# Kernel tuning notes

Measured on AMD Instinct MI355X. Metric: run time of the kernel, lower is better.

## Reference

```python
import jax, jax.numpy as jnp
import numpy as np

H = 4  # num_heads
EPS = 1e-5


def setup_inputs() -> dict:
    key = jax.random.key(0)
    ks = jax.random.split(key, 12)
    N, C, E = 4096, 128, 131072
    x = jax.random.normal(ks[0], (N, C), dtype=jnp.float32)
    edge_index = jax.random.randint(ks[1], (2, E), 0, N, dtype=jnp.int64)
    # guarantee every row has at least one neighbor (self-loops) to avoid NaN softmax rows
    loops = jnp.arange(N, dtype=jnp.int64)
    edge_index = edge_index.at[0, :N].set(loops).at[1, :N].set(loops)
    s = 1.0 / np.sqrt(C)
    def lin(k):
        kw, kb = jax.random.split(k)
        return (jax.random.uniform(kw, (C, C), jnp.float32, -s, s),
                jax.random.uniform(kb, (C,), jnp.float32, -s, s))
    wq, bq = lin(ks[2]); wk, bk = lin(ks[3]); wv, bv = lin(ks[4]); wo, bo = lin(ks[5])
    gamma = jnp.ones((C,), jnp.float32)
    beta = jnp.zeros((C,), jnp.float32)
    return {"x": x, "edge_index": edge_index, "wq": wq, "bq": bq, "wk": wk, "bk": bk,
            "wv": wv, "bv": bv, "wo": wo, "bo": bo, "gamma": gamma, "beta": beta}


def reference(x, edge_index, wq, bq, wk, bk, wv, bv, wo, bo, gamma, beta):
    N, C = x.shape
    D = C // H
    q = (x @ wq.T + bq).reshape(N, H, D)
    k = (x @ wk.T + bk).reshape(N, H, D)
    v = (x @ wv.T + bv).reshape(N, H, D)
    scores = jnp.einsum('nhd,mhd->nhm', q, k) / jnp.sqrt(jnp.float32(D))  # [N,H,N]
    row, col = edge_index
    mask = jnp.zeros((N, N), jnp.float32).at[row, col].set(1.0)
    scores = jnp.where(mask[:, None, :] == 0, -jnp.inf, scores)
    attn = jax.nn.softmax(scores, axis=-1)  # dropout is identity in eval
    out = jnp.einsum('nhm,mhd->nhd', attn, v).reshape(N, C)
    out = out @ wo.T + bo
    y = x + out
    mu = jnp.mean(y, axis=-1, keepdims=True)
    var = jnp.var(y, axis=-1, keepdims=True)
    return (y - mu) / jnp.sqrt(var + EPS) * gamma + beta
```

## Files before the change

### kernel.cpp

```cpp
#include <hip/hip_runtime.h>

typedef unsigned long long u64;

#define C_DIM 128
#define MAXN 128
#define WSTR (C_DIM + 4)

__global__ __launch_bounds__(512, 4) void build_qkv_kernel(
    const int* __restrict__ ei, int E, u64* __restrict__ bm, int wpr,
    const float* __restrict__ x,
    const float* __restrict__ wq, const float* __restrict__ bq,
    const float* __restrict__ wk, const float* __restrict__ bk,
    const float* __restrict__ wv, const float* __restrict__ bv,
    const float* __restrict__ wo, float* __restrict__ woT,
    float* __restrict__ qo, float* __restrict__ ko, float* __restrict__ vo)
{
    const int ROWS = 8;
    __shared__ float xs[ROWS][C_DIM];
    __shared__ float wt[C_DIM * WSTR];
    int t = threadIdx.x;
    int n0 = blockIdx.x * ROWS;
    int tid = blockIdx.x * 512 + t;
    int nth = gridDim.x * 512;

    if (tid < E) {
        int r = ei[tid], c = ei[E + tid];
        atomicOr(&bm[(size_t)r * wpr + (c >> 6)], 1ull << (c & 63));
    }
    for (int i = tid; i < C_DIM * C_DIM; i += nth) {
        int c = i >> 7, j = i & 127;
        woT[i] = wo[j * C_DIM + c];
    }

    if (t < 256) {
        int r = t >> 5, c4 = (t & 31) << 2;
        *(float4*)&xs[r][c4] = *(const float4*)(x + (size_t)(n0 + r) * C_DIM + c4);
    }
    int row = t >> 6;
    int jg  = t & 63;
    const float* Wp[3] = {wq, wk, wv};
    const float* Bp[3] = {bq, bk, bv};
    float*       Op[3] = {qo, ko, vo};
    for (int s = 0; s < 3; ++s) {
        __syncthreads();
        const float* W = Wp[s];
        #pragma unroll
        for (int i = 0; i < 8; ++i) {
            int g = t + i * 512;
            int j = g >> 5, c4 = (g & 31) << 2;
            *(float4*)&wt[j * WSTR + c4] = *(const float4*)(W + (size_t)j * C_DIM + c4);
        }
        __syncthreads();
        const float* B = Bp[s];
        float acc0 = B[jg], acc1 = B[jg + 64];
        for (int c = 0; c < C_DIM; c += 4) {
            float4 xa = *(const float4*)&xs[row][c];
            float4 w0 = *(const float4*)&wt[jg * WSTR + c];
            float4 w1 = *(const float4*)&wt[(jg + 64) * WSTR + c];
            acc0 += w0.x * xa.x + w0.y * xa.y + w0.z * xa.z + w0.w * xa.w;
            acc1 += w1.x * xa.x + w1.y * xa.y + w1.z * xa.z + w1.w * xa.w;
        }
        float* O = Op[s];
        size_t o = (size_t)(n0 + row) * C_DIM;
        O[o + jg]      = acc0;
        O[o + jg + 64] = acc1;
    }
}

__global__ __launch_bounds__(512, 4) void attn_oln_kernel(
    const float* __restrict__ q, const float* __restrict__ k,
    const float* __restrict__ v, const u64* __restrict__ bm, int wpr,
    const float* __restrict__ x,
    const float* __restrict__ woT, const float* __restrict__ bo,
    const float* __restrict__ gamma, const float* __restrict__ beta,
    float* __restrict__ out)
{
    const int ROWS = 8;
    __shared__ float qs[ROWS][C_DIM];
    __shared__ float xs[ROWS][C_DIM];
    __shared__ int   lm[ROWS][MAXN];
    __shared__ float ls[ROWS][4][MAXN];
    int t = threadIdx.x;
    int n0 = blockIdx.x * ROWS;
    int wave = t >> 6, lane = t & 63;
    const float scale = 0.17677669529663687f;

    int n = n0 + wave;
    qs[wave][lane]      = q[(size_t)n * C_DIM + lane] * scale;
    qs[wave][64 + lane] = q[(size_t)n * C_DIM + 64 + lane] * scale;
    u64 bits = bm[(size_t)n * wpr + lane];
    int pc = __popcll(bits);
    int incl = pc;
    #pragma unroll
    for (int off = 1; off < 64; off <<= 1) {
        int tv = __shfl_up(incl, off);
        if (lane >= off) incl += tv;
    }
    int cnt = __shfl(incl, 63);
    int pos = incl - pc;
    u64 bb = bits;
    while (bb) {
        int b = __builtin_ctzll(bb);
        bb &= bb - 1;
        if (pos < MAXN) lm[wave][pos] = (lane << 6) + b;
        ++pos;
    }
    if (cnt > MAXN) cnt = MAXN;
    __syncthreads();
    {
        int nb = lane & 15, hh = lane >> 4;
        float4 qf[8];
        #pragma unroll
        for (int u = 0; u < 8; ++u)
            qf[u] = *(const float4*)&qs[wave][hh * 32 + u * 4];
        for (int j0 = 0; j0 < cnt; j0 += 16) {
            int jj = j0 + nb;
            if (jj < cnt) {
                const float* kr = k + (size_t)lm[wave][jj] * C_DIM + hh * 32;
                float s = 0.f;
                #pragma unroll
                for (int u = 0; u < 8; ++u) {
                    float4 k4 = *(const float4*)(kr + u * 4);
                    s += qf[u].x * k4.x + qf[u].y * k4.y
                       + qf[u].z * k4.z + qf[u].w * k4.w;
                }
                ls[wave][hh][jj] = s;
            }
        }
    }
    __syncthreads();
    int g = lane >> 4, li = lane & 15;
    float mx = -1e30f;
    for (int jj = li; jj < cnt; jj += 16) mx = fmaxf(mx, ls[wave][g][jj]);
    #pragma unroll
    for (int off = 8; off; off >>= 1) mx = fmaxf(mx, __shfl_xor(mx, off));
    float sum = 0.f;
    for (int jj = li; jj < cnt; jj += 16) {
        float e = __expf(ls[wave][g][jj] - mx);
        ls[wave][g][jj] = e;
        sum += e;
    }
    #pragma unroll
    for (int off = 8; off; off >>= 1) sum += __shfl_xor(sum, off);
    float sinv = 1.0f / sum;
    __syncthreads();
    int h0 = lane >> 5;
    float s0 = __shfl(sinv, h0 * 16);
    float s1 = __shfl(sinv, (h0 + 2) * 16);
    float a0 = 0.f, a1 = 0.f;
    for (int j0 = 0; j0 < cnt; j0 += 16) {
        int cc = cnt - j0; if (cc > 16) cc = 16;
        float v0a[16], v1a[16];
        #pragma unroll
        for (int u = 0; u < 16; ++u) {
            if (u < cc) {
                int m = lm[wave][j0 + u];
                v0a[u] = v[(size_t)m * C_DIM + lane];
                v1a[u] = v[(size_t)m * C_DIM + 64 + lane];
            }
        }
        #pragma unroll
        for (int u = 0; u < 16; ++u) {
            if (u < cc) {
                a0 += ls[wave][h0][j0 + u] * v0a[u];
                a1 += ls[wave][h0 + 2][j0 + u] * v1a[u];
            }
        }
    }
    xs[wave][lane]      = a0 * s0;
    xs[wave][64 + lane] = a1 * s1;
    __syncthreads();
    int r  = t >> 6;
    int j2 = (t & 63) << 1;
    float2 acc = *(const float2*)(bo + j2);
    #pragma unroll 2
    for (int c = 0; c < C_DIM; c += 4) {
        #pragma unroll
        for (int u = 0; u < 4; ++u) {
            float2 w2 = *(const float2*)(woT + (size_t)(c + u) * C_DIM + j2);
            float xv = xs[r][c + u];
            acc.x += xv * w2.x;
            acc.y += xv * w2.y;
        }
    }
    __syncthreads();
    {
        float2 xr = *(const float2*)(x + (size_t)(n0 + r) * C_DIM + j2);
        xs[r][j2]     = acc.x + xr.x;
        xs[r][j2 + 1] = acc.y + xr.y;
    }
    __syncthreads();
    {
        float y0 = xs[wave][lane], y1 = xs[wave][64 + lane];
        float s = y0 + y1, s2 = y0 * y0 + y1 * y1;
        #pragma unroll
        for (int off = 32; off; off >>= 1) {
            s  += __shfl_xor(s, off);
            s2 += __shfl_xor(s2, off);
        }
        float mu = s * (1.0f / 128.0f);
        float var = s2 * (1.0f / 128.0f) - mu * mu;
        float rstd = rsqrtf(var + 1e-5f);
        size_t o = (size_t)n * C_DIM;
        out[o + lane]      = (y0 - mu) * rstd * gamma[lane] + beta[lane];
        out[o + 64 + lane] = (y1 - mu) * rstd * gamma[64 + lane] + beta[64 + lane];
    }
}

extern "C" void kernel_launch(void* const* d_in, const int* in_sizes, int n_in,
                              void* d_out, int out_size, void* d_ws, size_t ws_size,
                              hipStream_t stream)
{
    const float* x     = (const float*)d_in[0];
    const int*   ei    = (const int*)d_in[1];
    const float* wq    = (const float*)d_in[2];
    const float* bq    = (const float*)d_in[3];
    const float* wk    = (const float*)d_in[4];
    const float* bk    = (const float*)d_in[5];
    const float* wv    = (const float*)d_in[6];
    const float* bv    = (const float*)d_in[7];
    const float* wo    = (const float*)d_in[8];
    const float* bo    = (const float*)d_in[9];
    const float* gamma = (const float*)d_in[10];
    const float* beta  = (const float*)d_in[11];
    float* out = (float*)d_out;

    int N = in_sizes[0] / C_DIM;
    int E = in_sizes[1] / 2;
    int wpr = N >> 6;

    size_t mat_bytes = (size_t)N * C_DIM * sizeof(float);
    char* base = (char*)d_ws;
    float* q   = (float*)(base);
    float* k   = (float*)(base + mat_bytes);
    float* v   = (float*)(base + 2 * mat_bytes);
    u64*   bm  = (u64*)(base + 3 * mat_bytes);
    float* woT = (float*)(base + 4 * mat_bytes);

    hipMemsetAsync(bm, 0, (size_t)N * wpr * sizeof(u64), stream);
    build_qkv_kernel<<<N / 8, 512, 0, stream>>>(ei, E, bm, wpr,
                                                x, wq, bq, wk, bk, wv, bv,
                                                wo, woT, q, k, v);
    attn_oln_kernel<<<N / 8, 512, 0, stream>>>(q, k, v, bm, wpr,
                                               x, woT, bo, gamma, beta, out);
}
```

Measured before the change: 133.1 us.

## Compute QKV projection with split-bf16 MFMA instead of scalar FP32

Adds a prep kernel that builds the edge bitmask, transposes wo, and splits x and the QKV weights into high and low bf16 parts. A new kernel then computes the Q/K/V projections with 16x16x32 bf16 MFMA using three products (hh, hl, lh) to keep near-FP32 accuracy. This replaces the scalar FP32 LDS-tiled GEMM, which had a shared-memory weight reload per block. The cost is an extra kernel launch, extra global traffic for the split operands, and a small precision loss from dropping the low*low term.

```diff
diff --git a/kernel.cpp b/kernel.cpp
--- a/kernel.cpp
+++ b/kernel.cpp
@@ -1,69 +1,107 @@
 #include <hip/hip_runtime.h>
 
 typedef unsigned long long u64;
+typedef unsigned short u16;
+typedef __attribute__((ext_vector_type(8))) short short8;
+typedef __attribute__((ext_vector_type(4))) float f32x4;
 
 #define C_DIM 128
 #define MAXN 128
-#define WSTR (C_DIM + 4)
-
-__global__ __launch_bounds__(512, 4) void build_qkv_kernel(
+
+__device__ inline u16 bf16_rn(float f) {
+    unsigned u = __float_as_uint(f);
+    u += 0x7FFF + ((u >> 16) & 1);
+    return (u16)(u >> 16);
+}
+__device__ inline float bf16_tof(u16 h) { return __uint_as_float(((unsigned)h) << 16); }
+
+__global__ __launch_bounds__(256) void prep_kernel(
     const int* __restrict__ ei, int E, u64* __restrict__ bm, int wpr,
-    const float* __restrict__ x,
-    const float* __restrict__ wq, const float* __restrict__ bq,
-    const float* __restrict__ wk, const float* __restrict__ bk,
-    const float* __restrict__ wv, const float* __restrict__ bv,
-    const float* __restrict__ wo, float* __restrict__ woT,
-    float* __restrict__ qo, float* __restrict__ ko, float* __restrict__ vo)
-{
-    const int ROWS = 8;
-    __shared__ float xs[ROWS][C_DIM];
-    __shared__ float wt[C_DIM * WSTR];
-    int t = threadIdx.x;
-    int n0 = blockIdx.x * ROWS;
-    int tid = blockIdx.x * 512 + t;
-    int nth = gridDim.x * 512;
-
+    const float* __restrict__ x, u16* __restrict__ xh, u16* __restrict__ xl, int xq,
+    const float* __restrict__ wq, const float* __restrict__ wk, const float* __restrict__ wv,
+    u16* __restrict__ wH, u16* __restrict__ wL,
+    const float* __restrict__ wo, float* __restrict__ woT)
+{
+    int tid = blockIdx.x * 256 + threadIdx.x;
     if (tid < E) {
         int r = ei[tid], c = ei[E + tid];
         atomicOr(&bm[(size_t)r * wpr + (c >> 6)], 1ull << (c & 63));
     }
-    for (int i = tid; i < C_DIM * C_DIM; i += nth) {
-        int c = i >> 7, j = i & 127;
-        woT[i] = wo[j * C_DIM + c];
-    }
-
-    if (t < 256) {
-        int r = t >> 5, c4 = (t & 31) << 2;
-        *(float4*)&xs[r][c4] = *(const float4*)(x + (size_t)(n0 + r) * C_DIM + c4);
-    }
-    int row = t >> 6;
-    int jg  = t & 63;
-    const float* Wp[3] = {wq, wk, wv};
-    const float* Bp[3] = {bq, bk, bv};
-    float*       Op[3] = {qo, ko, vo};
-    for (int s = 0; s < 3; ++s) {
-        __syncthreads();
-        const float* W = Wp[s];
-        #pragma unroll
-        for (int i = 0; i < 8; ++i) {
-            int g = t + i * 512;
-            int j = g >> 5, c4 = (g & 31) << 2;
-            *(float4*)&wt[j * WSTR + c4] = *(const float4*)(W + (size_t)j * C_DIM + c4);
-        }
-        __syncthreads();
-        const float* B = Bp[s];
-        float acc0 = B[jg], acc1 = B[jg + 64];
-        for (int c = 0; c < C_DIM; c += 4) {
-            float4 xa = *(const float4*)&xs[row][c];
-            float4 w0 = *(const float4*)&wt[jg * WSTR + c];
-            float4 w1 = *(const float4*)&wt[(jg + 64) * WSTR + c];
-            acc0 += w0.x * xa.x + w0.y * xa.y + w0.z * xa.z + w0.w * xa.w;
-            acc1 += w1.x * xa.x + w1.y * xa.y + w1.z * xa.z + w1.w * xa.w;
-        }
-        float* O = Op[s];
-        size_t o = (size_t)(n0 + row) * C_DIM;
-        O[o + jg]      = acc0;
-        O[o + jg + 64] = acc1;
+    if (tid < C_DIM * C_DIM) {
+        int c = tid >> 7, j = tid & 127;
+        woT[tid] = wo[j * C_DIM + c];
+    }
+    if (tid < 3 * C_DIM * C_DIM) {
+        int s = tid >> 14, i = tid & 16383;
+        const float* W = (s == 0) ? wq : (s == 1) ? wk : wv;
+        float f = W[i];
+        u16 h = bf16_rn(f);
+        wH[tid] = h;
+        wL[tid] = bf16_rn(f - bf16_tof(h));
+    }
+    if (tid < xq) {
+        float4 xv = ((const float4*)x)[tid];
+        ushort4 h, l;
+        h.x = bf16_rn(xv.x); l.x = bf16_rn(xv.x - bf16_tof(h.x));
+        h.y = bf16_rn(xv.y); l.y = bf16_rn(xv.y - bf16_tof(h.y));
+        h.z = bf16_rn(xv.z); l.z = bf16_rn(xv.z - bf16_tof(h.z));
+        h.w = bf16_rn(xv.w); l.w = bf16_rn(xv.w - bf16_tof(h.w));
+        ((ushort4*)xh)[tid] = h;
+        ((ushort4*)xl)[tid] = l;
+    }
+}
+
+__global__ __launch_bounds__(256) void qkv_mfma_kernel(
+    const u16* __restrict__ xh, const u16* __restrict__ xl,
+    const u16* __restrict__ wH, const u16* __restrict__ wL,
+    const float* __restrict__ bq, const float* __restrict__ bk, const float* __restrict__ bv,
+    float* __restrict__ qo, float* __restrict__ ko, float* __restrict__ vo, int nrg)
+{
+    int bid = blockIdx.x;
+    int s = bid / nrg;
+    int rg = bid % nrg;
+    int r0 = rg * 16;
+    int w  = threadIdx.x >> 6;
+    int l  = threadIdx.x & 63;
+    int j0 = w * 32;
+    int lr = l & 15;
+    int kg = l >> 4;
+
+    const u16* xhp = xh + (size_t)(r0 + lr) * C_DIM + kg * 8;
+    const u16* xlp = xl + (size_t)(r0 + lr) * C_DIM + kg * 8;
+    const u16* wh  = wH + (size_t)s * C_DIM * C_DIM;
+    const u16* wl  = wL + (size_t)s * C_DIM * C_DIM;
+    const u16* w0h = wh + (size_t)(j0 + lr) * C_DIM + kg * 8;
+    const u16* w0l = wl + (size_t)(j0 + lr) * C_DIM + kg * 8;
+    const u16* w1h = w0h + 16 * C_DIM;
+    const u16* w1l = w0l + 16 * C_DIM;
+    const float* B = (s == 0) ? bq : (s == 1) ? bk : bv;
+    float*       O = (s == 0) ? qo : (s == 1) ? ko : vo;
+
+    float b0 = B[j0 + lr], b1 = B[j0 + 16 + lr];
+    f32x4 acc0 = {b0, b0, b0, b0};
+    f32x4 acc1 = {b1, b1, b1, b1};
+
+    #pragma unroll
+    for (int kk = 0; kk < C_DIM; kk += 32) {
+        short8 ah  = *(const short8*)(xhp + kk);
+        short8 al  = *(const short8*)(xlp + kk);
+        short8 bh0 = *(const short8*)(w0h + kk);
+        short8 bl0 = *(const short8*)(w0l + kk);
+        short8 bh1 = *(const short8*)(w1h + kk);
+        short8 bl1 = *(const short8*)(w1l + kk);
+        acc0 = __builtin_amdgcn_mfma_f32_16x16x32_bf16(ah, bh0, acc0, 0, 0, 0);
+        acc0 = __builtin_amdgcn_mfma_f32_16x16x32_bf16(ah, bl0, acc0, 0, 0, 0);
+        acc0 = __builtin_amdgcn_mfma_f32_16x16x32_bf16(al, bh0, acc0, 0, 0, 0);
+        acc1 = __builtin_amdgcn_mfma_f32_16x16x32_bf16(ah, bh1, acc1, 0, 0, 0);
+        acc1 = __builtin_amdgcn_mfma_f32_16x16x32_bf16(ah, bl1, acc1, 0, 0, 0);
+        acc1 = __builtin_amdgcn_mfma_f32_16x16x32_bf16(al, bh1, acc1, 0, 0, 0);
+    }
+    size_t ob = (size_t)(r0 + kg * 4) * C_DIM;
+    #pragma unroll
+    for (int i = 0; i < 4; ++i) {
+        O[ob + (size_t)i * C_DIM + j0 + lr]      = acc0[i];
+        O[ob + (size_t)i * C_DIM + j0 + 16 + lr] = acc1[i];
     }
 }
 
@@ -229,18 +267,29 @@
     int E = in_sizes[1] / 2;
     int wpr = N >> 6;
 
-    size_t mat_bytes = (size_t)N * C_DIM * sizeof(float);
+    size_t MB = 1 << 20;
     char* base = (char*)d_ws;
-    float* q   = (float*)(base);
-    float* k   = (float*)(base + mat_bytes);
-    float* v   = (float*)(base + 2 * mat_bytes);
-    u64*   bm  = (u64*)(base + 3 * mat_bytes);
-    float* woT = (float*)(base + 4 * mat_bytes);
+    float* q   = (float*)(base + 0 * MB);
+    float* k   = (float*)(base + 2 * MB);
+    float* v   = (float*)(base + 4 * MB);
+    u64*   bm  = (u64*)(base + 6 * MB);
+    float* woT = (float*)(base + 8 * MB);
+    u16*   xh  = (u16*)(base + 9 * MB);
+    u16*   xl  = (u16*)(base + 10 * MB);
+    u16*   wH  = (u16*)(base + 11 * MB);
+    u16*   wL  = (u16*)(base + 11 * MB + 512 * 1024);
 
     hipMemsetAsync(bm, 0, (size_t)N * wpr * sizeof(u64), stream);
-    build_qkv_kernel<<<N / 8, 512, 0, stream>>>(ei, E, bm, wpr,
-                                                x, wq, bq, wk, bk, wv, bv,
-                                                wo, woT, q, k, v);
+
+    int xq = N * C_DIM / 4;
+    int nwork = (E > xq) ? E : xq;
+    prep_kernel<<<(nwork + 255) / 256, 256, 0, stream>>>(
+        ei, E, bm, wpr, x, xh, xl, xq, wq, wk, wv, wH, wL, wo, woT);
+
+    int nrg = N / 16;
+    qkv_mfma_kernel<<<3 * nrg, 256, 0, stream>>>(
+        xh, xl, wH, wL, bq, bk, bv, q, k, v, nrg);
+
     attn_oln_kernel<<<N / 8, 512, 0, stream>>>(q, k, v, bm, wpr,
                                                x, woT, bo, gamma, beta, out);
 }
```

Measured after the change: 130.5 us. -2.0%, faster.
